# Performance work log

Hardware: AMD Instinct MI355X
Metric: run time of the kernel (lower is better)

Reference implementation:

```python
import jax, jax.numpy as jnp
import numpy as np
from jax import lax

B, C, HID, H, W = 8, 256, 64, 64, 64

def conv3x3(x, w, b):
    # x: [B,C_in,H,W], w: [C_out,C_in,3,3], b: [C_out]
    y = lax.conv_general_dilated(x, w, window_strides=(1, 1), padding='SAME',
                                 dimension_numbers=('NCHW', 'OIHW', 'NCHW'))
    return y + b[None, :, None, None]

def setup_inputs() -> dict:
    key = jax.random.key(0)
    ks = jax.random.split(key, 7)
    s_in = 1.0 / np.sqrt(C * 9)
    return {
        'x': jax.random.normal(ks[0], (B, C, H, W), dtype=jnp.float32),
        'Wq': jax.random.normal(ks[1], (HID, C, 3, 3), dtype=jnp.float32) * s_in,
        'bq': jax.random.normal(ks[2], (HID,), dtype=jnp.float32) * s_in,
        'Wk': jax.random.normal(ks[3], (HID, C, 3, 3), dtype=jnp.float32) * s_in,
        'bk': jax.random.normal(ks[4], (HID,), dtype=jnp.float32) * s_in,
        'Wv': jax.random.normal(ks[5], (C, C, 3, 3), dtype=jnp.float32) * s_in,
        'bv': jax.random.normal(ks[6], (C,), dtype=jnp.float32) * s_in,
    }

def reference(x, Wq, bq, Wk, bk, Wv, bv):
    b, c, w, h = x.shape
    n = w * h
    q = conv3x3(x, Wq, bq).reshape(b, -1, n).transpose(0, 2, 1)  # [B,N,hid]
    k = conv3x3(x, Wk, bk).reshape(b, -1, n)                      # [B,hid,N]
    v = conv3x3(x, Wv, bv).reshape(b, c, n)                       # [B,C,N]
    attn = jax.nn.softmax(jnp.einsum('bnd,bdm->bnm', q, k), axis=-1)  # [B,N,N]
    # out = bmm(value, attn^T): out[b,c,m] = sum_n v[b,c,n] * attn[b,m,n]
    out = jnp.einsum('bcn,bmn->bcm', v, attn).reshape(b, c, w, h)
    # F.interpolate(out, h, mode='bilinear') with H==W is an exact identity
    return out + x
```

## Files before the change

### kernel.cpp

```cpp
#include <hip/hip_runtime.h>
#include <math.h>

#define NB   8
#define NC   256
#define ND   64
#define NPIX 4096
#define LSTR 72

typedef short bf16x8 __attribute__((ext_vector_type(8)));
typedef float f32x4  __attribute__((ext_vector_type(4)));
typedef float f32x16 __attribute__((ext_vector_type(16)));

static __device__ __forceinline__ ushort f2bf(float f) {
    uint u = __float_as_uint(f);
    u += 0x7fffu + ((u >> 16) & 1u);
    return (ushort)(u >> 16);
}
static __device__ __forceinline__ float bf2f(ushort h) {
    return __uint_as_float(((uint)h) << 16);
}

__global__ __launch_bounds__(256) void transpose_x(
    const float* __restrict__ x, ushort* __restrict__ xth, ushort* __restrict__ xtl)
{
    __shared__ float tile[64][68];
    const int t = threadIdx.x;
    const int p0 = blockIdx.x * 64, c0 = blockIdx.y * 64, b = blockIdx.z;

    const int cl = t >> 4, p4 = (t & 15) * 4;
    #pragma unroll
    for (int i = 0; i < 4; i++) {
        const int c = cl + 16 * i;
        *(float4*)&tile[c][p4] =
            *(const float4*)&x[((size_t)(b * NC + c0 + c)) * NPIX + p0 + p4];
    }
    __syncthreads();

    const int pl = t & 63, ch = t >> 6;
    float v[16];
    #pragma unroll
    for (int j = 0; j < 16; j++) v[j] = tile[ch * 16 + j][pl];
    ushort h[16], l[16];
    #pragma unroll
    for (int j = 0; j < 16; j++) {
        h[j] = f2bf(v[j]);
        l[j] = f2bf(v[j] - bf2f(h[j]));
    }
    const size_t o = ((size_t)(b * NPIX + p0 + pl)) * 256 + c0 + ch * 16;
    *(uint4*)&xth[o]     = *(uint4*)&h[0];
    *(uint4*)&xth[o + 8] = *(uint4*)&h[8];
    *(uint4*)&xtl[o]     = *(uint4*)&l[0];
    *(uint4*)&xtl[o + 8] = *(uint4*)&l[8];
}

__global__ __launch_bounds__(256) void transpose_w(
    const float* __restrict__ Wq, const float* __restrict__ Wk,
    const float* __restrict__ Wv,
    ushort* __restrict__ qh, ushort* __restrict__ ql,
    ushort* __restrict__ kh, ushort* __restrict__ kl,
    ushort* __restrict__ vh)
{
    __shared__ float wb[2304];
    const int g = blockIdx.x, t = threadIdx.x;
    const float* src;
    ushort *dh, *dl;
    int co, Co, split;
    if (g < 64)       { src = Wq + (size_t)g * 2304; co = g;       Co = 64;  dh = qh; dl = ql; split = 1; }
    else if (g < 128) { src = Wk + (size_t)(g - 64) * 2304; co = g - 64; Co = 64; dh = kh; dl = kl; split = 1; }
    else              { src = Wv + (size_t)(g - 128) * 2304; co = g - 128; Co = 256; dh = vh; dl = nullptr; split = 0; }

    for (int i = t; i < 2304; i += 256) wb[i] = src[i];
    __syncthreads();
    for (int j = t; j < 2304; j += 256) {
        const int rs = j >> 8, ci = j & 255;
        const float v = wb[ci * 9 + rs];
        const ushort hv = f2bf(v);
        const size_t o = ((size_t)(rs * Co + co)) * 256 + ci;
        dh[o] = hv;
        if (split) dl[o] = f2bf(v - bf2f(hv));
    }
}

__global__ __launch_bounds__(256) void conv_qk_k(
    const ushort* __restrict__ xth, const ushort* __restrict__ xtl,
    const ushort* __restrict__ wqh, const ushort* __restrict__ wql,
    const ushort* __restrict__ wkh, const ushort* __restrict__ wkl,
    const float* __restrict__ bq, const float* __restrict__ bk,
    ushort* __restrict__ qoh, ushort* __restrict__ qol,
    ushort* __restrict__ koh, ushort* __restrict__ kol)
{
    extern __shared__ char smem[];
    ushort* xs = (ushort*)smem;
    float*  sbias = (float*)(smem + 76032);

    const int hq = blockIdx.x, b = blockIdx.y, ct = blockIdx.z;
    const ushort* wth = ct ? wkh : wqh;
    const ushort* wtl = ct ? wkl : wql;
    const float*  bias = ct ? bk : bq;
    ushort* outh = ct ? koh : qoh;
    ushort* outl = ct ? kol : qol;

    const int t = threadIdx.x;
    const int wv = t >> 6, lane = t & 63;
    const int l31 = lane & 31, khl = lane >> 5;
    const int lanebase = l31 * 24 + khl * 8;
    const int h = hq * 4 + wv;

    if (t < 64) sbias[t] = bias[t];
    for (int i = t; i < 768; i += 256) {
        const int buf = i / 384, rem = i % 384;
        const int p = rem / 192, r2 = rem % 192;
        const int row = r2 / 32, e = (r2 % 32) / 16, ci = r2 & 15;
        xs[(size_t)(buf * 2 + p) * 9504 + (row * 66 + e * 65) * 24 + ci] = 0;
    }

    int s_cih[3], s_col[3], s_row[3], s_hs[3];
    #pragma unroll
    for (int i = 0; i < 3; i++) {
        const int a = i * 256 + t;
        s_cih[i] = a & 1; s_col[i] = (a >> 1) & 63; s_row[i] = a >> 7;
        s_hs[i] = hq * 4 + s_row[i] - 1;
    }

    uint4 xr[6];
    #pragma unroll
    for (int i = 0; i < 3; i++) {
        uint4 vh = {0,0,0,0}, vl = {0,0,0,0};
        if (s_hs[i] >= 0 && s_hs[i] < 64) {
            const size_t g = ((size_t)(b * NPIX + s_hs[i] * 64 + s_col[i])) * 256 + s_cih[i] * 8;
            vh = *(const uint4*)&xth[g];
            vl = *(const uint4*)&xtl[g];
        }
        xr[i] = vh; xr[3 + i] = vl;
    }
    #pragma unroll
    for (int i = 0; i < 3; i++) {
        const size_t o = (s_row[i] * 66 + 1 + s_col[i]) * 24 + s_cih[i] * 8;
        *(uint4*)&xs[o]                   = xr[i];
        *(uint4*)&xs[(size_t)9504 + o]    = xr[3 + i];
    }
    __syncthreads();

    f32x16 a00 = {0}, a01 = {0}, a10 = {0}, a11 = {0};

    for (int ch = 0; ch < 16; ch++) {
        const int cur = ch & 1, ci0 = ch * 16;
        if (ch < 15) {
            const int ci1 = ci0 + 16;
            #pragma unroll
            for (int i = 0; i < 3; i++) {
                uint4 vh = {0,0,0,0}, vl = {0,0,0,0};
                if (s_hs[i] >= 0 && s_hs[i] < 64) {
                    const size_t g = ((size_t)(b * NPIX + s_hs[i] * 64 + s_col[i])) * 256 + ci1 + s_cih[i] * 8;
                    vh = *(const uint4*)&xth[g];
                    vl = *(const uint4*)&xtl[g];
                }
                xr[i] = vh; xr[3 + i] = vl;
            }
        }
        const ushort* xh = xs + (size_t)(cur * 2 + 0) * 9504;
        const ushort* xl = xs + (size_t)(cur * 2 + 1) * 9504;
        #pragma unroll
        for (int rs = 0; rs < 9; rs++) {
            const int r = rs / 3, s = rs % 3;
            bf16x8 A0h = *(const bf16x8*)&wth[((size_t)(rs * 64 + l31)) * 256 + ci0 + khl * 8];
            bf16x8 A1h = *(const bf16x8*)&wth[((size_t)(rs * 64 + 32 + l31)) * 256 + ci0 + khl * 8];
            bf16x8 A0l = *(const bf16x8*)&wtl[((size_t)(rs * 64 + l31)) * 256 + ci0 + khl * 8];
            bf16x8 A1l = *(const bf16x8*)&wtl[((size_t)(rs * 64 + 32 + l31)) * 256 + ci0 + khl * 8];
            const int xo = ((wv + r) * 66 + s) * 24 + lanebase;
            bf16x8 B0h = *(const bf16x8*)&xh[xo];
            bf16x8 B1h = *(const bf16x8*)&xh[xo + 768];
            bf16x8 B0l = *(const bf16x8*)&xl[xo];
            bf16x8 B1l = *(const bf16x8*)&xl[xo + 768];
            a00 = __builtin_amdgcn_mfma_f32_32x32x16_bf16(A0h, B0h, a00, 0, 0, 0);
            a01 = __builtin_amdgcn_mfma_f32_32x32x16_bf16(A0h, B1h, a01, 0, 0, 0);
            a10 = __builtin_amdgcn_mfma_f32_32x32x16_bf16(A1h, B0h, a10, 0, 0, 0);
            a11 = __builtin_amdgcn_mfma_f32_32x32x16_bf16(A1h, B1h, a11, 0, 0, 0);
            a00 = __builtin_amdgcn_mfma_f32_32x32x16_bf16(A0l, B0h, a00, 0, 0, 0);
            a01 = __builtin_amdgcn_mfma_f32_32x32x16_bf16(A0l, B1h, a01, 0, 0, 0);
            a10 = __builtin_amdgcn_mfma_f32_32x32x16_bf16(A1l, B0h, a10, 0, 0, 0);
            a11 = __builtin_amdgcn_mfma_f32_32x32x16_bf16(A1l, B1h, a11, 0, 0, 0);
            a00 = __builtin_amdgcn_mfma_f32_32x32x16_bf16(A0h, B0l, a00, 0, 0, 0);
            a01 = __builtin_amdgcn_mfma_f32_32x32x16_bf16(A0h, B1l, a01, 0, 0, 0);
            a10 = __builtin_amdgcn_mfma_f32_32x32x16_bf16(A1h, B0l, a10, 0, 0, 0);
            a11 = __builtin_amdgcn_mfma_f32_32x32x16_bf16(A1h, B1l, a11, 0, 0, 0);
        }
        if (ch < 15) {
            const int nb = cur ^ 1;
            #pragma unroll
            for (int i = 0; i < 3; i++) {
                const size_t o = (size_t)(nb * 2) * 9504 + (s_row[i] * 66 + 1 + s_col[i]) * 24 + s_cih[i] * 8;
                *(uint4*)&xs[o]        = xr[i];
                *(uint4*)&xs[o + 9504] = xr[3 + i];
            }
        }
        __syncthreads();
    }

    const float4* sb4 = (const float4*)sbias;
    #pragma unroll
    for (int ms = 0; ms < 2; ms++)
        #pragma unroll
        for (int ns = 0; ns < 2; ns++) {
            const f32x16 av = ms ? (ns ? a11 : a10) : (ns ? a01 : a00);
            const int p = h * 64 + ns * 32 + l31;
            #pragma unroll
            for (int g = 0; g < 4; g++) {
                const float4 bi = sb4[ms * 8 + 2 * g + khl];
                float v0 = av[4 * g + 0] + bi.x;
                float v1 = av[4 * g + 1] + bi.y;
                float v2 = av[4 * g + 2] + bi.z;
                float v3 = av[4 * g + 3] + bi.w;
                ushort4 hv, lv;
                hv.x = f2bf(v0); lv.x = f2bf(v0 - bf2f(hv.x));
                hv.y = f2bf(v1); lv.y = f2bf(v1 - bf2f(hv.y));
                hv.z = f2bf(v2); lv.z = f2bf(v2 - bf2f(hv.z));
                hv.w = f2bf(v3); lv.w = f2bf(v3 - bf2f(hv.w));
                const size_t o = ((size_t)(b * NPIX + p)) * 64 + ms * 32 + 8 * g + 4 * khl;
                *(ushort4*)&outh[o] = hv;
                *(ushort4*)&outl[o] = lv;
            }
        }
}

__global__ __launch_bounds__(256) void conv_v_k(
    const ushort* __restrict__ xth, const ushort* __restrict__ wtv,
    const float* __restrict__ bv, ushort* __restrict__ vout)
{
    extern __shared__ char smem[];
    ushort* xs = (ushort*)smem;
    float*  sbias = (float*)(smem + 38016);

    const int hq = blockIdx.x, b = blockIdx.y, co0 = blockIdx.z * 64;
    const int t = threadIdx.x;
    const int wv = t >> 6, lane = t & 63;
    const int l31 = lane & 31, khl = lane >> 5;
    const int lanebase = l31 * 24 + khl * 8;
    const int h = hq * 4 + wv;

    if (t < 64) sbias[t] = bv[co0 + t];
    for (int i = t; i < 384; i += 256) {
        const int buf = i / 192, r2 = i % 192;
        const int row = r2 / 32, e = (r2 % 32) / 16, ci = r2 & 15;
        xs[(size_t)buf * 9504 + (row * 66 + e * 65) * 24 + ci] = 0;
    }

    int s_cih[3], s_col[3], s_row[3], s_hs[3];
    #pragma unroll
    for (int i = 0; i < 3; i++) {
        const int a = i * 256 + t;
        s_cih[i] = a & 1; s_col[i] = (a >> 1) & 63; s_row[i] = a >> 7;
        s_hs[i] = hq * 4 + s_row[i] - 1;
    }

    uint4 xr[3];
    #pragma unroll
    for (int i = 0; i < 3; i++) {
        uint4 vh = {0,0,0,0};
        if (s_hs[i] >= 0 && s_hs[i] < 64)
            vh = *(const uint4*)&xth[((size_t)(b * NPIX + s_hs[i] * 64 + s_col[i])) * 256 + s_cih[i] * 8];
        xr[i] = vh;
    }
    #pragma unroll
    for (int i = 0; i < 3; i++)
        *(uint4*)&xs[(s_row[i] * 66 + 1 + s_col[i]) * 24 + s_cih[i] * 8] = xr[i];
    __syncthreads();

    f32x16 a00 = {0}, a01 = {0}, a10 = {0}, a11 = {0};

    for (int ch = 0; ch < 16; ch++) {
        const int cur = ch & 1, ci0 = ch * 16;
        if (ch < 15) {
            const int ci1 = ci0 + 16;
            #pragma unroll
            for (int i = 0; i < 3; i++) {
                uint4 vh = {0,0,0,0};
                if (s_hs[i] >= 0 && s_hs[i] < 64)
                    vh = *(const uint4*)&xth[((size_t)(b * NPIX + s_hs[i] * 64 + s_col[i])) * 256 + ci1 + s_cih[i] * 8];
                xr[i] = vh;
            }
        }
        const ushort* xh = xs + (size_t)cur * 9504;
        #pragma unroll
        for (int rs = 0; rs < 9; rs++) {
            const int r = rs / 3, s = rs % 3;
            const int xo = ((wv + r) * 66 + s) * 24 + lanebase;
            bf16x8 A0 = *(const bf16x8*)&xh[xo];
            bf16x8 A1 = *(const bf16x8*)&xh[xo + 768];
            bf16x8 B0 = *(const bf16x8*)&wtv[((size_t)(rs * 256 + co0 + l31)) * 256 + ci0 + khl * 8];
            bf16x8 B1 = *(const bf16x8*)&wtv[((size_t)(rs * 256 + co0 + 32 + l31)) * 256 + ci0 + khl * 8];
            a00 = __builtin_amdgcn_mfma_f32_32x32x16_bf16(A0, B0, a00, 0, 0, 0);
            a01 = __builtin_amdgcn_mfma_f32_32x32x16_bf16(A0, B1, a01, 0, 0, 0);
            a10 = __builtin_amdgcn_mfma_f32_32x32x16_bf16(A1, B0, a10, 0, 0, 0);
            a11 = __builtin_amdgcn_mfma_f32_32x32x16_bf16(A1, B1, a11, 0, 0, 0);
        }
        if (ch < 15) {
            const int nb = cur ^ 1;
            #pragma unroll
            for (int i = 0; i < 3; i++)
                *(uint4*)&xs[(size_t)nb * 9504 + (s_row[i] * 66 + 1 + s_col[i]) * 24 + s_cih[i] * 8] = xr[i];
        }
        __syncthreads();
    }

    #pragma unroll
    for (int ns = 0; ns < 2; ns++) {
        const int co = co0 + ns * 32 + l31;
        const float bi = sbias[ns * 32 + l31];
        #pragma unroll
        for (int ms = 0; ms < 2; ms++) {
            const f32x16 av = ms ? (ns ? a11 : a10) : (ns ? a01 : a00);
            #pragma unroll
            for (int g = 0; g < 4; g++) {
                const int p = h * 64 + ms * 32 + 8 * g + 4 * khl;
                ushort4 ov;
                ov.x = f2bf(av[4 * g + 0] + bi);
                ov.y = f2bf(av[4 * g + 1] + bi);
                ov.z = f2bf(av[4 * g + 2] + bi);
                ov.w = f2bf(av[4 * g + 3] + bi);
                *(ushort4*)&vout[((size_t)(b * NC + co)) * NPIX + p] = ov;
            }
        }
    }
}

__global__ __launch_bounds__(512, 2) void attn_k(
    const ushort* __restrict__ qh, const ushort* __restrict__ ql,
    const ushort* __restrict__ kh, const ushort* __restrict__ kl,
    const ushort* __restrict__ vb, const float* __restrict__ x,
    float* __restrict__ out)
{
    const int b    = blockIdx.y;
    const int m0   = blockIdx.x * 128;
    const int t    = threadIdx.x;
    const int wave = t >> 6;
    const int lane = t & 63;
    const int quad = lane >> 4;
    const int l16  = lane & 15;

    extern __shared__ char smem[];
    ushort* skh = (ushort*)(smem);
    ushort* skl = (ushort*)(smem + 18432);
    ushort* sps = (ushort*)(smem + 36864);
    float*  red = (float*)(smem + 55296);
    float*  ivl = (float*)(smem + 57344);

    const int mgbase = 2 * (wave & 3);
    const int ntbase = 2 * (wave >> 2);
    bf16x8 aqh[2][2], aql[2][2];
    #pragma unroll
    for (int mgi = 0; mgi < 2; mgi++)
        #pragma unroll
        for (int ks = 0; ks < 2; ks++) {
            const size_t g = ((size_t)b * NPIX + m0 + 16 * (mgbase + mgi) + l16) * ND + 32 * ks + quad * 8;
            aqh[mgi][ks] = *(const bf16x8*)&qh[g];
            aql[mgi][ks] = *(const bf16x8*)&ql[g];
        }

    const int krow = t >> 3, kseg = (t & 7) * 8;
    {
        const size_t g = ((size_t)b * NPIX + krow) * ND + kseg;
        *(uint4*)&skh[krow * LSTR + kseg] = *(const uint4*)&kh[g];
        *(uint4*)&skl[krow * LSTR + kseg] = *(const uint4*)&kl[g];
    }

    f32x4 acc[8][2];
    #pragma unroll
    for (int i = 0; i < 8; i++)
        #pragma unroll
        for (int j = 0; j < 2; j++) acc[i][j] = (f32x4){0.f, 0.f, 0.f, 0.f};
    float rsum = 0.f;
    const int rs_row = t & 127, rs_co = (t >> 7) * 16;
    __syncthreads();

    for (int n0 = 0; n0 < NPIX; n0 += 64) {
        const int cur = (n0 >> 6) & 1, nxt = cur ^ 1;

        bf16x8 vf[2][2];
        #pragma unroll
        for (int ct = 0; ct < 2; ct++)
            #pragma unroll
            for (int ks = 0; ks < 2; ks++) {
                const int c = 32 * wave + 16 * ct + l16;
                vf[ct][ks] = *(const bf16x8*)&vb[((size_t)b * NC + c) * NPIX + n0 + 32 * ks + quad * 8];
            }
        uint4 knh = {0,0,0,0}, knl = {0,0,0,0};
        const bool have_next = (n0 + 64) < NPIX;
        if (have_next) {
            const size_t g = ((size_t)b * NPIX + n0 + 64 + krow) * ND + kseg;
            knh = *(const uint4*)&kh[g];
            knl = *(const uint4*)&kl[g];
        }

        #pragma unroll
        for (int nti = 0; nti < 2; nti++) {
            const int nt = ntbase + nti;
            bf16x8 bh[2], bl[2];
            #pragma unroll
            for (int ks = 0; ks < 2; ks++) {
                const int o = cur * 4608 + (16 * nt + l16) * LSTR + 32 * ks + quad * 8;
                bh[ks] = *(const bf16x8*)&skh[o];
                bl[ks] = *(const bf16x8*)&skl[o];
            }
            #pragma unroll
            for (int mgi = 0; mgi < 2; mgi++) {
                f32x4 s = {0.f, 0.f, 0.f, 0.f};
                #pragma unroll
                for (int ks = 0; ks < 2; ks++) {
                    s = __builtin_amdgcn_mfma_f32_16x16x32_bf16(aqh[mgi][ks], bh[ks], s, 0, 0, 0);
                    s = __builtin_amdgcn_mfma_f32_16x16x32_bf16(aql[mgi][ks], bh[ks], s, 0, 0, 0);
                    s = __builtin_amdgcn_mfma_f32_16x16x32_bf16(aqh[mgi][ks], bl[ks], s, 0, 0, 0);
                }
                #pragma unroll
                for (int r = 0; r < 4; r++) {
                    const float p = __expf(s[r] - 30.f);
                    sps[(16 * (mgbase + mgi) + quad * 4 + r) * LSTR + 16 * nt + l16] = f2bf(p);
                }
            }
        }
        if (have_next) {
            *(uint4*)&skh[nxt * 4608 + krow * LSTR + kseg] = knh;
            *(uint4*)&skl[nxt * 4608 + krow * LSTR + kseg] = knl;
        }
        __syncthreads();

        {
            uint4 p0 = *(const uint4*)&sps[rs_row * LSTR + rs_co];
            uint4 p1 = *(const uint4*)&sps[rs_row * LSTR + rs_co + 8];
            const ushort* pu0 = (const ushort*)&p0;
            const ushort* pu1 = (const ushort*)&p1;
            float ss = 0.f;
            #pragma unroll
            for (int i = 0; i < 8; i++) ss += bf2f(pu0[i]) + bf2f(pu1[i]);
            rsum += ss;
        }

        #pragma unroll
        for (int ks = 0; ks < 2; ks++) {
            bf16x8 ap[8];
            #pragma unroll
            for (int mg = 0; mg < 8; mg++)
                ap[mg] = *(const bf16x8*)&sps[(16 * mg + l16) * LSTR + 32 * ks + quad * 8];
            #pragma unroll
            for (int mg = 0; mg < 8; mg++)
                #pragma unroll
                for (int ct = 0; ct < 2; ct++)
                    acc[mg][ct] = __builtin_amdgcn_mfma_f32_16x16x32_bf16(
                        ap[mg], vf[ct][ks], acc[mg][ct], 0, 0, 0);
        }
        __syncthreads();
    }

    red[rs_row * 4 + (t >> 7)] = rsum;
    __syncthreads();
    if (t < 128)
        ivl[t] = 1.f / (red[t * 4 + 0] + red[t * 4 + 1] + red[t * 4 + 2] + red[t * 4 + 3]);
    __syncthreads();

    #pragma unroll
    for (int mg = 0; mg < 8; mg++) {
        const int mrow = 16 * mg + quad * 4;
        const float4 il4 = *(const float4*)&ivl[mrow];
        const int m = m0 + mrow;
        #pragma unroll
        for (int ct = 0; ct < 2; ct++) {
            const int c = 32 * wave + 16 * ct + l16;
            const size_t base = ((size_t)b * NC + c) * NPIX + m;
            const float4 xv = *(const float4*)&x[base];
            const f32x4 a = acc[mg][ct];
            float4 o;
            o.x = fmaf(a[0], il4.x, xv.x);
            o.y = fmaf(a[1], il4.y, xv.y);
            o.z = fmaf(a[2], il4.z, xv.z);
            o.w = fmaf(a[3], il4.w, xv.w);
            *(float4*)&out[base] = o;
        }
    }
}

extern "C" void kernel_launch(void* const* d_in, const int* in_sizes, int n_in,
                              void* d_out, int out_size, void* d_ws, size_t ws_size,
                              hipStream_t stream)
{
    const float* x  = (const float*)d_in[0];
    const float* Wq = (const float*)d_in[1];
    const float* bq = (const float*)d_in[2];
    const float* Wk = (const float*)d_in[3];
    const float* bk = (const float*)d_in[4];
    const float* Wv = (const float*)d_in[5];
    const float* bv = (const float*)d_in[6];
    float* outp = (float*)d_out;

    const size_t XT = (size_t)NB * NPIX * 256;
    const size_t QK = (size_t)NB * NPIX * ND;
    ushort* xt_h = (ushort*)d_ws;
    ushort* xt_l = xt_h + XT;
    ushort* v_b  = xt_l;
    ushort* q_h  = xt_l + XT;
    ushort* q_l  = q_h + QK;
    ushort* k_h  = q_l + QK;
    ushort* k_l  = k_h + QK;
    ushort* wtq_h = k_l + QK;
    ushort* wtq_l = wtq_h + 147456;
    ushort* wtk_h = wtq_l + 147456;
    ushort* wtk_l = wtk_h + 147456;
    ushort* wtv_h = wtk_l + 147456;

    dim3 blk(256);
    transpose_x<<<dim3(64, 4, NB), blk, 0, stream>>>(x, xt_h, xt_l);
    transpose_w<<<dim3(384), blk, 0, stream>>>(Wq, Wk, Wv, wtq_h, wtq_l, wtk_h, wtk_l, wtv_h);
    conv_qk_k<<<dim3(16, NB, 2), blk, 76288, stream>>>(
        xt_h, xt_l, wtq_h, wtq_l, wtk_h, wtk_l, bq, bk, q_h, q_l, k_h, k_l);
    conv_v_k<<<dim3(16, NB, 4), blk, 38272, stream>>>(xt_h, wtv_h, bv, v_b);
    attn_k<<<dim3(32, NB), dim3(512), 57856, stream>>>(q_h, q_l, k_h, k_l, v_b, x, outp);
}
```

Before: 438.0 us.

## Stage conv weights in LDS and retile attention to 64-query blocks

Both conv kernels now stage the per-chunk weight tiles in shared memory, register-prefetched from global, instead of each wave reading weights directly from global memory. The x tile drops from double to single buffering with two barriers per chunk, and occupancy hints are added. The attention kernel is retiled to 256-thread blocks over 64 query rows, reading K fragments straight from global and computing row sums in registers with shuffles. This aims to cut redundant global weight traffic and raise occupancy, at the cost of more barriers and uncached K reloads per block.

Measured after the change: 457.7 us. +4.5%, slower.

```diff
diff --git a/kernel.cpp b/kernel.cpp
--- a/kernel.cpp
+++ b/kernel.cpp
@@ -81,7 +81,7 @@
     }
 }
 
-__global__ __launch_bounds__(256) void conv_qk_k(
+__global__ __launch_bounds__(256, 2) void conv_qk_k(
     const ushort* __restrict__ xth, const ushort* __restrict__ xtl,
     const ushort* __restrict__ wqh, const ushort* __restrict__ wql,
     const ushort* __restrict__ wkh, const ushort* __restrict__ wkl,
@@ -89,9 +89,9 @@
     ushort* __restrict__ qoh, ushort* __restrict__ qol,
     ushort* __restrict__ koh, ushort* __restrict__ kol)
 {
-    extern __shared__ char smem[];
-    ushort* xs = (ushort*)smem;
-    float*  sbias = (float*)(smem + 76032);
+    __shared__ ushort xs[2][6 * 66 * 24];
+    __shared__ ushort ws[9 * 2 * 64 * 16];
+    __shared__ float  sbias[64];
 
     const int hq = blockIdx.x, b = blockIdx.y, ct = blockIdx.z;
     const ushort* wth = ct ? wkh : wqh;
@@ -103,15 +103,13 @@
     const int t = threadIdx.x;
     const int wv = t >> 6, lane = t & 63;
     const int l31 = lane & 31, khl = lane >> 5;
-    const int lanebase = l31 * 24 + khl * 8;
     const int h = hq * 4 + wv;
 
     if (t < 64) sbias[t] = bias[t];
-    for (int i = t; i < 768; i += 256) {
-        const int buf = i / 384, rem = i % 384;
-        const int p = rem / 192, r2 = rem % 192;
+    for (int i = t; i < 384; i += 256) {
+        const int p = i / 192, r2 = i % 192;
         const int row = r2 / 32, e = (r2 % 32) / 16, ci = r2 & 15;
-        xs[(size_t)(buf * 2 + p) * 9504 + (row * 66 + e * 65) * 24 + ci] = 0;
+        xs[p][(row * 66 + e * 65) * 24 + ci] = 0;
     }
 
     int s_cih[3], s_col[3], s_row[3], s_hs[3];
@@ -121,8 +119,14 @@
         s_cih[i] = a & 1; s_col[i] = (a >> 1) & 63; s_row[i] = a >> 7;
         s_hs[i] = hq * 4 + s_row[i] - 1;
     }
-
-    uint4 xr[6];
+    int w_cih[9], w_co[9], w_hl[9], w_rs[9];
+    #pragma unroll
+    for (int i = 0; i < 9; i++) {
+        const int a = i * 256 + t;
+        w_cih[i] = a & 1; w_co[i] = (a >> 1) & 63; w_hl[i] = (a >> 7) & 1; w_rs[i] = a >> 8;
+    }
+
+    uint4 xr[6], wr[9];
     #pragma unroll
     for (int i = 0; i < 3; i++) {
         uint4 vh = {0,0,0,0}, vl = {0,0,0,0};
@@ -134,19 +138,29 @@
         xr[i] = vh; xr[3 + i] = vl;
     }
     #pragma unroll
-    for (int i = 0; i < 3; i++) {
-        const size_t o = (s_row[i] * 66 + 1 + s_col[i]) * 24 + s_cih[i] * 8;
-        *(uint4*)&xs[o]                   = xr[i];
-        *(uint4*)&xs[(size_t)9504 + o]    = xr[3 + i];
-    }
-    __syncthreads();
+    for (int i = 0; i < 9; i++) {
+        const ushort* wsrc = w_hl[i] ? wtl : wth;
+        wr[i] = *(const uint4*)&wsrc[((size_t)(w_rs[i] * 64 + w_co[i])) * 256 + w_cih[i] * 8];
+    }
 
     f32x16 a00 = {0}, a01 = {0}, a10 = {0}, a11 = {0};
+    const int wAbase = l31 * 16 + khl * 8;
+    const int xBbase = khl * 8;
 
     for (int ch = 0; ch < 16; ch++) {
-        const int cur = ch & 1, ci0 = ch * 16;
+        #pragma unroll
+        for (int i = 0; i < 3; i++) {
+            const int o = (s_row[i] * 66 + 1 + s_col[i]) * 24 + s_cih[i] * 8;
+            *(uint4*)&xs[0][o] = xr[i];
+            *(uint4*)&xs[1][o] = xr[3 + i];
+        }
+        #pragma unroll
+        for (int i = 0; i < 9; i++)
+            *(uint4*)&ws[((w_rs[i] * 2 + w_hl[i]) * 64 + w_co[i]) * 16 + w_cih[i] * 8] = wr[i];
+        __syncthreads();
+
         if (ch < 15) {
-            const int ci1 = ci0 + 16;
+            const int ci1 = (ch + 1) * 16;
             #pragma unroll
             for (int i = 0; i < 3; i++) {
                 uint4 vh = {0,0,0,0}, vl = {0,0,0,0};
@@ -157,21 +171,25 @@
                 }
                 xr[i] = vh; xr[3 + i] = vl;
             }
-        }
-        const ushort* xh = xs + (size_t)(cur * 2 + 0) * 9504;
-        const ushort* xl = xs + (size_t)(cur * 2 + 1) * 9504;
+            #pragma unroll
+            for (int i = 0; i < 9; i++) {
+                const ushort* wsrc = w_hl[i] ? wtl : wth;
+                wr[i] = *(const uint4*)&wsrc[((size_t)(w_rs[i] * 64 + w_co[i])) * 256 + ci1 + w_cih[i] * 8];
+            }
+        }
+
         #pragma unroll
         for (int rs = 0; rs < 9; rs++) {
             const int r = rs / 3, s = rs % 3;
-            bf16x8 A0h = *(const bf16x8*)&wth[((size_t)(rs * 64 + l31)) * 256 + ci0 + khl * 8];
-            bf16x8 A1h = *(const bf16x8*)&wth[((size_t)(rs * 64 + 32 + l31)) * 256 + ci0 + khl * 8];
-            bf16x8 A0l = *(const bf16x8*)&wtl[((size_t)(rs * 64 + l31)) * 256 + ci0 + khl * 8];
-            bf16x8 A1l = *(const bf16x8*)&wtl[((size_t)(rs * 64 + 32 + l31)) * 256 + ci0 + khl * 8];
-            const int xo = ((wv + r) * 66 + s) * 24 + lanebase;
-            bf16x8 B0h = *(const bf16x8*)&xh[xo];
-            bf16x8 B1h = *(const bf16x8*)&xh[xo + 768];
-            bf16x8 B0l = *(const bf16x8*)&xl[xo];
-            bf16x8 B1l = *(const bf16x8*)&xl[xo + 768];
+            bf16x8 A0h = *(const bf16x8*)&ws[(rs * 2 + 0) * 1024 + wAbase];
+            bf16x8 A1h = *(const bf16x8*)&ws[(rs * 2 + 0) * 1024 + 512 + wAbase];
+            bf16x8 A0l = *(const bf16x8*)&ws[(rs * 2 + 1) * 1024 + wAbase];
+            bf16x8 A1l = *(const bf16x8*)&ws[(rs * 2 + 1) * 1024 + 512 + wAbase];
+            const int xo = ((wv + r) * 66 + s + l31) * 24 + xBbase;
+            bf16x8 B0h = *(const bf16x8*)&xs[0][xo];
+            bf16x8 B1h = *(const bf16x8*)&xs[0][xo + 768];
+            bf16x8 B0l = *(const bf16x8*)&xs[1][xo];
+            bf16x8 B1l = *(const bf16x8*)&xs[1][xo + 768];
             a00 = __builtin_amdgcn_mfma_f32_32x32x16_bf16(A0h, B0h, a00, 0, 0, 0);
             a01 = __builtin_amdgcn_mfma_f32_32x32x16_bf16(A0h, B1h, a01, 0, 0, 0);
             a10 = __builtin_amdgcn_mfma_f32_32x32x16_bf16(A1h, B0h, a10, 0, 0, 0);
@@ -184,15 +202,6 @@
             a01 = __builtin_amdgcn_mfma_f32_32x32x16_bf16(A0h, B1l, a01, 0, 0, 0);
             a10 = __builtin_amdgcn_mfma_f32_32x32x16_bf16(A1h, B0l, a10, 0, 0, 0);
             a11 = __builtin_amdgcn_mfma_f32_32x32x16_bf16(A1h, B1l, a11, 0, 0, 0);
-        }
-        if (ch < 15) {
-            const int nb = cur ^ 1;
-            #pragma unroll
-            for (int i = 0; i < 3; i++) {
-                const size_t o = (size_t)(nb * 2) * 9504 + (s_row[i] * 66 + 1 + s_col[i]) * 24 + s_cih[i] * 8;
-                *(uint4*)&xs[o]        = xr[i];
-                *(uint4*)&xs[o + 9504] = xr[3 + i];
-            }
         }
         __syncthreads();
     }
@@ -223,26 +232,24 @@
         }
 }
 
-__global__ __launch_bounds__(256) void conv_v_k(
+__global__ __launch_bounds__(256, 2) void conv_v_k(
     const ushort* __restrict__ xth, const ushort* __restrict__ wtv,
     const float* __restrict__ bv, ushort* __restrict__ vout)
 {
-    extern __shared__ char smem[];
-    ushort* xs = (ushort*)smem;
-    float*  sbias = (float*)(smem + 38016);
+    __shared__ ushort xs[6 * 66 * 24];
+    __shared__ ushort ws[9 * 64 * 16];
+    __shared__ float  sbias[64];
 
     const int hq = blockIdx.x, b = blockIdx.y, co0 = blockIdx.z * 64;
     const int t = threadIdx.x;
     const int wv = t >> 6, lane = t & 63;
     const int l31 = lane & 31, khl = lane >> 5;
-    const int lanebase = l31 * 24 + khl * 8;
     const int h = hq * 4 + wv;
 
     if (t < 64) sbias[t] = bv[co0 + t];
-    for (int i = t; i < 384; i += 256) {
-        const int buf = i / 192, r2 = i % 192;
-        const int row = r2 / 32, e = (r2 % 32) / 16, ci = r2 & 15;
-        xs[(size_t)buf * 9504 + (row * 66 + e * 65) * 24 + ci] = 0;
+    for (int i = t; i < 192; i += 256) {
+        const int row = i / 32, e = (i % 32) / 16, ci = i & 15;
+        xs[(row * 66 + e * 65) * 24 + ci] = 0;
     }
 
     int s_cih[3], s_col[3], s_row[3], s_hs[3];
@@ -252,8 +259,16 @@
         s_cih[i] = a & 1; s_col[i] = (a >> 1) & 63; s_row[i] = a >> 7;
         s_hs[i] = hq * 4 + s_row[i] - 1;
     }
-
-    uint4 xr[3];
+    int w_cih[5], w_co[5], w_rs[5], w_ok[5];
+    #pragma unroll
+    for (int i = 0; i < 5; i++) {
+        const int a = i * 256 + t;
+        w_ok[i] = a < 1152;
+        const int aa = w_ok[i] ? a : 0;
+        w_cih[i] = aa & 1; w_co[i] = (aa >> 1) & 63; w_rs[i] = aa >> 7;
+    }
+
+    uint4 xr[3], wr[5];
     #pragma unroll
     for (int i = 0; i < 3; i++) {
         uint4 vh = {0,0,0,0};
@@ -262,16 +277,26 @@
         xr[i] = vh;
     }
     #pragma unroll
-    for (int i = 0; i < 3; i++)
-        *(uint4*)&xs[(s_row[i] * 66 + 1 + s_col[i]) * 24 + s_cih[i] * 8] = xr[i];
-    __syncthreads();
+    for (int i = 0; i < 5; i++)
+        if (w_ok[i])
+            wr[i] = *(const uint4*)&wtv[((size_t)(w_rs[i] * 256 + co0 + w_co[i])) * 256 + w_cih[i] * 8];
 
     f32x16 a00 = {0}, a01 = {0}, a10 = {0}, a11 = {0};
+    const int wBbase = l31 * 16 + khl * 8;
+    const int xAbase = khl * 8;
 
     for (int ch = 0; ch < 16; ch++) {
-        const int cur = ch & 1, ci0 = ch * 16;
+        #pragma unroll
+        for (int i = 0; i < 3; i++)
+            *(uint4*)&xs[(s_row[i] * 66 + 1 + s_col[i]) * 24 + s_cih[i] * 8] = xr[i];
+        #pragma unroll
+        for (int i = 0; i < 5; i++)
+            if (w_ok[i])
+                *(uint4*)&ws[(w_rs[i] * 64 + w_co[i]) * 16 + w_cih[i] * 8] = wr[i];
+        __syncthreads();
+
         if (ch < 15) {
-            const int ci1 = ci0 + 16;
+            const int ci1 = (ch + 1) * 16;
             #pragma unroll
             for (int i = 0; i < 3; i++) {
                 uint4 vh = {0,0,0,0};
@@ -279,26 +304,24 @@
                     vh = *(const uint4*)&xth[((size_t)(b * NPIX + s_hs[i] * 64 + s_col[i])) * 256 + ci1 + s_cih[i] * 8];
                 xr[i] = vh;
             }
-        }
-        const ushort* xh = xs + (size_t)cur * 9504;
+            #pragma unroll
+            for (int i = 0; i < 5; i++)
+                if (w_ok[i])
+                    wr[i] = *(const uint4*)&wtv[((size_t)(w_rs[i] * 256 + co0 + w_co[i])) * 256 + ci1 + w_cih[i] * 8];
+        }
+
         #pragma unroll
         for (int rs = 0; rs < 9; rs++) {
             const int r = rs / 3, s = rs % 3;
-            const int xo = ((wv + r) * 66 + s) * 24 + lanebase;
-            bf16x8 A0 = *(const bf16x8*)&xh[xo];
-            bf16x8 A1 = *(const bf16x8*)&xh[xo + 768];
-            bf16x8 B0 = *(const bf16x8*)&wtv[((size_t)(rs * 256 + co0 + l31)) * 256 + ci0 + khl * 8];
-            bf16x8 B1 = *(const bf16x8*)&wtv[((size_t)(rs * 256 + co0 + 32 + l31)) * 256 + ci0 + khl * 8];
+            const int xo = ((wv + r) * 66 + s + l31) * 24 + xAbase;
+            bf16x8 A0 = *(const bf16x8*)&xs[xo];
+            bf16x8 A1 = *(const bf16x8*)&xs[xo + 768];
+            bf16x8 B0 = *(const bf16x8*)&ws[rs * 1024 + wBbase];
+            bf16x8 B1 = *(const bf16x8*)&ws[rs * 1024 + 512 + wBbase];
             a00 = __builtin_amdgcn_mfma_f32_32x32x16_bf16(A0, B0, a00, 0, 0, 0);
             a01 = __builtin_amdgcn_mfma_f32_32x32x16_bf16(A0, B1, a01, 0, 0, 0);
             a10 = __builtin_amdgcn_mfma_f32_32x32x16_bf16(A1, B0, a10, 0, 0, 0);
             a11 = __builtin_amdgcn_mfma_f32_32x32x16_bf16(A1, B1, a11, 0, 0, 0);
-        }
-        if (ch < 15) {
-            const int nb = cur ^ 1;
-            #pragma unroll
-            for (int i = 0; i < 3; i++)
-                *(uint4*)&xs[(size_t)nb * 9504 + (s_row[i] * 66 + 1 + s_col[i]) * 24 + s_cih[i] * 8] = xr[i];
         }
         __syncthreads();
     }
@@ -324,147 +347,122 @@
     }
 }
 
-__global__ __launch_bounds__(512, 2) void attn_k(
+__global__ __launch_bounds__(256, 2) void attn_k(
     const ushort* __restrict__ qh, const ushort* __restrict__ ql,
     const ushort* __restrict__ kh, const ushort* __restrict__ kl,
     const ushort* __restrict__ vb, const float* __restrict__ x,
     float* __restrict__ out)
 {
-    const int b    = blockIdx.y;
-    const int m0   = blockIdx.x * 128;
-    const int t    = threadIdx.x;
-    const int wave = t >> 6;
+    const int id = blockIdx.x;
+    const int b  = id & 7;
+    const int m0 = (id >> 3) * 64;
+    const int t  = threadIdx.x;
+    const int w  = t >> 6;
     const int lane = t & 63;
     const int quad = lane >> 4;
     const int l16  = lane & 15;
 
-    extern __shared__ char smem[];
-    ushort* skh = (ushort*)(smem);
-    ushort* skl = (ushort*)(smem + 18432);
-    ushort* sps = (ushort*)(smem + 36864);
-    float*  red = (float*)(smem + 55296);
-    float*  ivl = (float*)(smem + 57344);
-
-    const int mgbase = 2 * (wave & 3);
-    const int ntbase = 2 * (wave >> 2);
-    bf16x8 aqh[2][2], aql[2][2];
-    #pragma unroll
-    for (int mgi = 0; mgi < 2; mgi++)
+    __shared__ ushort sps[64 * LSTR];
+    __shared__ float  red[4][64];
+    __shared__ float  ivl[64];
+
+    bf16x8 aqh[4][2], aql[4][2];
+    #pragma unroll
+    for (int mg = 0; mg < 4; mg++)
         #pragma unroll
         for (int ks = 0; ks < 2; ks++) {
-            const size_t g = ((size_t)b * NPIX + m0 + 16 * (mgbase + mgi) + l16) * ND + 32 * ks + quad * 8;
-            aqh[mgi][ks] = *(const bf16x8*)&qh[g];
-            aql[mgi][ks] = *(const bf16x8*)&ql[g];
-        }
-
-    const int krow = t >> 3, kseg = (t & 7) * 8;
-    {
-        const size_t g = ((size_t)b * NPIX + krow) * ND + kseg;
-        *(uint4*)&skh[krow * LSTR + kseg] = *(const uint4*)&kh[g];
-        *(uint4*)&skl[krow * LSTR + kseg] = *(const uint4*)&kl[g];
-    }
-
-    f32x4 acc[8][2];
-    #pragma unroll
-    for (int i = 0; i < 8; i++)
-        #pragma unroll
-        for (int j = 0; j < 2; j++) acc[i][j] = (f32x4){0.f, 0.f, 0.f, 0.f};
-    float rsum = 0.f;
-    const int rs_row = t & 127, rs_co = (t >> 7) * 16;
-    __syncthreads();
+            const size_t g = ((size_t)b * NPIX + m0 + mg * 16 + l16) * ND + ks * 32 + quad * 8;
+            aqh[mg][ks] = *(const bf16x8*)&qh[g];
+            aql[mg][ks] = *(const bf16x8*)&ql[g];
+        }
+
+    f32x4 acc[4][4];
+    #pragma unroll
+    for (int i = 0; i < 4; i++)
+        #pragma unroll
+        for (int j = 0; j < 4; j++) acc[i][j] = (f32x4){0.f, 0.f, 0.f, 0.f};
+    float lsum[4] = {0.f, 0.f, 0.f, 0.f};
 
     for (int n0 = 0; n0 < NPIX; n0 += 64) {
-        const int cur = (n0 >> 6) & 1, nxt = cur ^ 1;
-
-        bf16x8 vf[2][2];
-        #pragma unroll
-        for (int ct = 0; ct < 2; ct++)
+        bf16x8 kfh[2], kfl[2];
+        #pragma unroll
+        for (int ks = 0; ks < 2; ks++) {
+            const size_t g = ((size_t)b * NPIX + n0 + 16 * w + l16) * ND + ks * 32 + quad * 8;
+            kfh[ks] = *(const bf16x8*)&kh[g];
+            kfl[ks] = *(const bf16x8*)&kl[g];
+        }
+        bf16x8 vf[4][2];
+        #pragma unroll
+        for (int ct = 0; ct < 4; ct++)
             #pragma unroll
             for (int ks = 0; ks < 2; ks++) {
-                const int c = 32 * wave + 16 * ct + l16;
-                vf[ct][ks] = *(const bf16x8*)&vb[((size_t)b * NC + c) * NPIX + n0 + 32 * ks + quad * 8];
-            }
-        uint4 knh = {0,0,0,0}, knl = {0,0,0,0};
-        const bool have_next = (n0 + 64) < NPIX;
-        if (have_next) {
-            const size_t g = ((size_t)b * NPIX + n0 + 64 + krow) * ND + kseg;
-            knh = *(const uint4*)&kh[g];
-            knl = *(const uint4*)&kl[g];
-        }
-
-        #pragma unroll
-        for (int nti = 0; nti < 2; nti++) {
-            const int nt = ntbase + nti;
-            bf16x8 bh[2], bl[2];
+                const int c = 64 * w + ct * 16 + l16;
+                vf[ct][ks] = *(const bf16x8*)&vb[((size_t)b * NC + c) * NPIX + n0 + ks * 32 + quad * 8];
+            }
+
+        #pragma unroll
+        for (int mg = 0; mg < 4; mg++) {
+            f32x4 s = {0.f, 0.f, 0.f, 0.f};
             #pragma unroll
             for (int ks = 0; ks < 2; ks++) {
-                const int o = cur * 4608 + (16 * nt + l16) * LSTR + 32 * ks + quad * 8;
-                bh[ks] = *(const bf16x8*)&skh[o];
-                bl[ks] = *(const bf16x8*)&skl[o];
-            }
-            #pragma unroll
-            for (int mgi = 0; mgi < 2; mgi++) {
-                f32x4 s = {0.f, 0.f, 0.f, 0.f};
+                s = __builtin_amdgcn_mfma_f32_16x16x32_bf16(kfh[ks], aqh[mg][ks], s, 0, 0, 0);
+                s = __builtin_amdgcn_mfma_f32_16x16x32_bf16(kfl[ks], aqh[mg][ks], s, 0, 0, 0);
+                s = __builtin_amdgcn_mfma_f32_16x16x32_bf16(kfh[ks], aql[mg][ks], s, 0, 0, 0);
+            }
+            uint2 pk;
+            float ss = 0.f;
+            {
+                const ushort p0 = f2bf(__expf(s[0] - 30.f));
+                const ushort p1 = f2bf(__expf(s[1] - 30.f));
+                const ushort p2 = f2bf(__expf(s[2] - 30.f));
+                const ushort p3 = f2bf(__expf(s[3] - 30.f));
+                ss = (bf2f(p0) + bf2f(p1)) + (bf2f(p2) + bf2f(p3));
+                pk.x = (uint)p0 | ((uint)p1 << 16);
+                pk.y = (uint)p2 | ((uint)p3 << 16);
+            }
+            lsum[mg] += ss;
+            *(uint2*)&sps[(mg * 16 + l16) * LSTR + 16 * w + quad * 4] = pk;
+        }
+        __syncthreads();
+
+        #pragma unroll
+        for (int ks = 0; ks < 2; ks++) {
+            bf16x8 ap[4];
+            #pragma unroll
+            for (int mg = 0; mg < 4; mg++)
+                ap[mg] = *(const bf16x8*)&sps[(mg * 16 + l16) * LSTR + ks * 32 + quad * 8];
+            #pragma unroll
+            for (int mg = 0; mg < 4; mg++)
                 #pragma unroll
-                for (int ks = 0; ks < 2; ks++) {
-                    s = __builtin_amdgcn_mfma_f32_16x16x32_bf16(aqh[mgi][ks], bh[ks], s, 0, 0, 0);
-                    s = __builtin_amdgcn_mfma_f32_16x16x32_bf16(aql[mgi][ks], bh[ks], s, 0, 0, 0);
-                    s = __builtin_amdgcn_mfma_f32_16x16x32_bf16(aqh[mgi][ks], bl[ks], s, 0, 0, 0);
-                }
-                #pragma unroll
-                for (int r = 0; r < 4; r++) {
-                    const float p = __expf(s[r] - 30.f);
-                    sps[(16 * (mgbase + mgi) + quad * 4 + r) * LSTR + 16 * nt + l16] = f2bf(p);
-                }
-            }
-        }
-        if (have_next) {
-            *(uint4*)&skh[nxt * 4608 + krow * LSTR + kseg] = knh;
-            *(uint4*)&skl[nxt * 4608 + krow * LSTR + kseg] = knl;
-        }
-        __syncthreads();
-
-        {
-            uint4 p0 = *(const uint4*)&sps[rs_row * LSTR + rs_co];
-            uint4 p1 = *(const uint4*)&sps[rs_row * LSTR + rs_co + 8];
-            const ushort* pu0 = (const ushort*)&p0;
-            const ushort* pu1 = (const ushort*)&p1;
-            float ss = 0.f;
-            #pragma unroll
-            for (int i = 0; i < 8; i++) ss += bf2f(pu0[i]) + bf2f(pu1[i]);
-            rsum += ss;
-        }
-
-        #pragma unroll
-        for (int ks = 0; ks < 2; ks++) {
-            bf16x8 ap[8];
-            #pragma unroll
-            for (int mg = 0; mg < 8; mg++)
-                ap[mg] = *(const bf16x8*)&sps[(16 * mg + l16) * LSTR + 32 * ks + quad * 8];
-            #pragma unroll
-            for (int mg = 0; mg < 8; mg++)
-                #pragma unroll
-                for (int ct = 0; ct < 2; ct++)
+                for (int ct = 0; ct < 4; ct++)
                     acc[mg][ct] = __builtin_amdgcn_mfma_f32_16x16x32_bf16(
                         ap[mg], vf[ct][ks], acc[mg][ct], 0, 0, 0);
         }
         __syncthreads();
     }
 
-    red[rs_row * 4 + (t >> 7)] = rsum;
+    #pragma unroll
+    for (int mg = 0; mg < 4; mg++) {
+        lsum[mg] += __shfl_xor(lsum[mg], 16, 64);
+        lsum[mg] += __shfl_xor(lsum[mg], 32, 64);
+    }
+    if (quad == 0) {
+        #pragma unroll
+        for (int mg = 0; mg < 4; mg++) red[w][mg * 16 + l16] = lsum[mg];
+    }
     __syncthreads();
-    if (t < 128)
-        ivl[t] = 1.f / (red[t * 4 + 0] + red[t * 4 + 1] + red[t * 4 + 2] + red[t * 4 + 3]);
+    if (t < 64)
+        ivl[t] = 1.f / (red[0][t] + red[1][t] + red[2][t] + red[3][t]);
     __syncthreads();
 
     #pragma unroll
-    for (int mg = 0; mg < 8; mg++) {
-        const int mrow = 16 * mg + quad * 4;
+    for (int mg = 0; mg < 4; mg++) {
+        const int mrow = mg * 16 + quad * 4;
         const float4 il4 = *(const float4*)&ivl[mrow];
         const int m = m0 + mrow;
         #pragma unroll
-        for (int ct = 0; ct < 2; ct++) {
-            const int c = 32 * wave + 16 * ct + l16;
+        for (int ct = 0; ct < 4; ct++) {
+            const int c = 64 * w + ct * 16 + l16;
             const size_t base = ((size_t)b * NC + c) * NPIX + m;
             const float4 xv = *(const float4*)&x[base];
             const f32x4 a = acc[mg][ct];
@@ -509,8 +507,8 @@
     dim3 blk(256);
     transpose_x<<<dim3(64, 4, NB), blk, 0, stream>>>(x, xt_h, xt_l);
     transpose_w<<<dim3(384), blk, 0, stream>>>(Wq, Wk, Wv, wtq_h, wtq_l, wtk_h, wtk_l, wtv_h);
-    conv_qk_k<<<dim3(16, NB, 2), blk, 76288, stream>>>(
+    conv_qk_k<<<dim3(16, NB, 2), blk, 0, stream>>>(
         xt_h, xt_l, wtq_h, wtq_l, wtk_h, wtk_l, bq, bk, q_h, q_l, k_h, k_l);
-    conv_v_k<<<dim3(16, NB, 4), blk, 38272, stream>>>(xt_h, wtv_h, bv, v_b);
-    attn_k<<<dim3(32, NB), dim3(512), 57856, stream>>>(q_h, q_l, k_h, k_l, v_b, x, outp);
-}
+    conv_v_k<<<dim3(16, NB, 4), blk, 0, stream>>>(xt_h, wtv_h, bv, v_b);
+    attn_k<<<dim3(512), blk, 0, stream>>>(q_h, q_l, k_h, k_l, v_b, x, outp);
+}
```
